# Kernel optimization log

Hardware: AMD Instinct MI355X
Metric: run time of the kernel (lower is better)

Reference implementation:

```python
import jax, jax.numpy as jnp
import numpy as np

TAU = 2.0     # membrane decay constant (init arg tau)
ALPHA = 1.0   # surrogate-gradient width (self.alpha() == 1.0)

# PiecewiseQuadratic surrogate spike: heaviside fwd, quadratic-band bwd
@jax.custom_vjp
def spike(v):
    return (v >= 0.0).astype(v.dtype)

def _spike_fwd(v):
    return spike(v), v

def _spike_bwd(v, g):
    sg = jnp.where(jnp.abs(v) > 1.0 / ALPHA, 0.0, -ALPHA * ALPHA * jnp.abs(v) + ALPHA)
    return (g * sg.astype(g.dtype),)

spike.defvjp(_spike_fwd, _spike_bwd)


def setup_inputs() -> dict:
    key = jax.random.key(0)
    x = jax.random.normal(key, (64, 64, 8192), dtype=jnp.float32)  # [B, T, F]
    return {
        "x": x,
        "momentum": jnp.array([0.9], dtype=jnp.float32),
        "lamb": jnp.array([0.5], dtype=jnp.float32),
        "thresholds": jnp.array([1.0], dtype=jnp.float32),
    }


def reference(x, momentum, lamb, thresholds):
    # regular=False -> lamb used directly (no sigmoid)
    mt = momentum[0]
    lb = lamb[0]
    th = thresholds[0]
    xt = jnp.moveaxis(x, 1, 0)  # [T, B, F] for scan over time
    u0 = jnp.zeros_like(xt[0])
    m0 = jnp.zeros_like(xt[0])

    def step(carry, xi):
        u_last, m = carry
        u = u_last / TAU + xi
        s = spike(u - th)
        m = mt * m + (1.0 - mt) * (u - u_last)
        u_next = (u * lb + m * (1.0 - lb)) * (1.0 - s)
        return (u_next, m), s

    _, out = jax.lax.scan(step, (u0, m0), xt)
    return jnp.moveaxis(out, 0, 1)  # [B, T, F]
```

## Files before the change

kernel.cpp:

```cpp
#include <hip/hip_runtime.h>


constexpr int B  = 64;
constexpr int T  = 64;
constexpr int F  = 8192;
constexpr int F2 = F / 2;
constexpr int P  = 4;

__global__ __launch_bounds__(256) void lif_fwd_kernel(
    const float2* __restrict__ x,
    const float*  __restrict__ momentum,
    const float*  __restrict__ lamb,
    const float*  __restrict__ thresholds,
    float2*       __restrict__ out)
{
#pragma clang fp contract(off)

    const int tid = blockIdx.x * blockDim.x + threadIdx.x;
    const int b   = tid / F2;
    const int f2  = tid - b * F2;

    const float mt  = momentum[0];
    const float omt = 1.0f - mt;
    const float lb  = lamb[0];
    const float olb = 1.0f - lb;
    const float th  = thresholds[0];

    const int base = b * (T * F2) + f2;

    float2 buf[P];
#pragma unroll
    for (int i = 0; i < P; ++i) buf[i] = x[base + i * F2];

    float u0 = 0.0f, u1 = 0.0f;
    float m0 = 0.0f, m1 = 0.0f;

    int load_idx  = base + P * F2;
    int store_idx = base;

#pragma unroll 4
    for (int t = 0; t < T; ++t) {
        const float2 xi = buf[t & (P - 1)];

        if (t + P < T) {
            buf[t & (P - 1)] = x[load_idx];
            load_idx += F2;
        }

        float2 sv;
        {
            const float u  = u0 * 0.5f + xi.x;
            const float s  = ((u - th) >= 0.0f) ? 1.0f : 0.0f;
            const float a  = mt * m0;
            const float bq = omt * (u - u0);
            m0 = a + bq;
            u0 = (u * lb + m0 * olb) * (1.0f - s);
            sv.x = s;
        }
        {
            const float u  = u1 * 0.5f + xi.y;
            const float s  = ((u - th) >= 0.0f) ? 1.0f : 0.0f;
            const float a  = mt * m1;
            const float bq = omt * (u - u1);
            m1 = a + bq;
            u1 = (u * lb + m1 * olb) * (1.0f - s);
            sv.y = s;
        }

        out[store_idx] = sv;
        store_idx += F2;
    }
}

extern "C" void kernel_launch(void* const* d_in, const int* in_sizes, int n_in,
                              void* d_out, int out_size, void* d_ws, size_t ws_size,
                              hipStream_t stream) {
    const float2* x   = (const float2*)d_in[0];
    const float*  mom = (const float*)d_in[1];
    const float*  lmb = (const float*)d_in[2];
    const float*  thr = (const float*)d_in[3];
    float2* out = (float2*)d_out;

    const int n_threads = B * F2;
    const int block = 256;
    const int grid = n_threads / block;
    lif_fwd_kernel<<<grid, block, 0, stream>>>(x, mom, lmb, thr, out);
}
```

Measured before the change: 242.7 us.

## Skew four batch chains per thread in staggered phases with nontemporal stores

Each thread now handles one feature across four batches. The four scan chains are offset in time by 16 steps and advanced in phased, fully unrolled loops, so independent recurrences interleave and more loads are in flight per thread. Accesses change from float2 to scalar float, and spike outputs are written with nontemporal stores to avoid polluting the cache. This cuts the thread count by a factor of four and raises register use, and scalar accesses may lower per-instruction memory efficiency.

```diff
diff --git a/kernel.cpp b/kernel.cpp
--- a/kernel.cpp
+++ b/kernel.cpp
@@ -1,24 +1,49 @@
 #include <hip/hip_runtime.h>
 
 
-constexpr int B  = 64;
-constexpr int T  = 64;
-constexpr int F  = 8192;
-constexpr int F2 = F / 2;
-constexpr int P  = 4;
+constexpr int B = 64;
+constexpr int T = 64;
+constexpr int F = 8192;
+constexpr int S   = 4;
+constexpr int DLT = 16;
+
+template <int GLO, int GHI>
+__device__ __forceinline__ void run_phase(
+    int tau0, const int* base, float* u, float* m,
+    const float* __restrict__ x, float* __restrict__ out,
+    float mt, float omt, float lb, float olb, float th)
+{
+#pragma clang fp contract(off)
+#pragma unroll
+    for (int k = 0; k < DLT; ++k) {
+        const int tau = tau0 + k;
+#pragma unroll
+        for (int g = GLO; g <= GHI; ++g) {
+            const int t   = tau - DLT * g;
+            const int idx = base[g] + t * F;
+            const float xv = x[idx];
+            const float uu = u[g] * 0.5f + xv;
+            const float s  = ((uu - th) >= 0.0f) ? 1.0f : 0.0f;
+            const float a  = mt * m[g];
+            const float bq = omt * (uu - u[g]);
+            m[g] = a + bq;
+            u[g] = (uu * lb + m[g] * olb) * (1.0f - s);
+            __builtin_nontemporal_store(s, &out[idx]);
+        }
+    }
+}
 
 __global__ __launch_bounds__(256) void lif_fwd_kernel(
-    const float2* __restrict__ x,
-    const float*  __restrict__ momentum,
-    const float*  __restrict__ lamb,
-    const float*  __restrict__ thresholds,
-    float2*       __restrict__ out)
+    const float* __restrict__ x,
+    const float* __restrict__ momentum,
+    const float* __restrict__ lamb,
+    const float* __restrict__ thresholds,
+    float*       __restrict__ out)
 {
 #pragma clang fp contract(off)
-
     const int tid = blockIdx.x * blockDim.x + threadIdx.x;
-    const int b   = tid / F2;
-    const int f2  = tid - b * F2;
+    const int b0  = tid >> 13;
+    const int f   = tid & (F - 1);
 
     const float mt  = momentum[0];
     const float omt = 1.0f - mt;
@@ -26,62 +51,34 @@
     const float olb = 1.0f - lb;
     const float th  = thresholds[0];
 
-    const int base = b * (T * F2) + f2;
+    int   base[S];
+    float u[S], m[S];
+#pragma unroll
+    for (int g = 0; g < S; ++g) {
+        base[g] = (b0 + 16 * g) * (T * F) + f;
+        u[g] = 0.0f;
+        m[g] = 0.0f;
+    }
 
-    float2 buf[P];
-#pragma unroll
-    for (int i = 0; i < P; ++i) buf[i] = x[base + i * F2];
-
-    float u0 = 0.0f, u1 = 0.0f;
-    float m0 = 0.0f, m1 = 0.0f;
-
-    int load_idx  = base + P * F2;
-    int store_idx = base;
-
-#pragma unroll 4
-    for (int t = 0; t < T; ++t) {
-        const float2 xi = buf[t & (P - 1)];
-
-        if (t + P < T) {
-            buf[t & (P - 1)] = x[load_idx];
-            load_idx += F2;
-        }
-
-        float2 sv;
-        {
-            const float u  = u0 * 0.5f + xi.x;
-            const float s  = ((u - th) >= 0.0f) ? 1.0f : 0.0f;
-            const float a  = mt * m0;
-            const float bq = omt * (u - u0);
-            m0 = a + bq;
-            u0 = (u * lb + m0 * olb) * (1.0f - s);
-            sv.x = s;
-        }
-        {
-            const float u  = u1 * 0.5f + xi.y;
-            const float s  = ((u - th) >= 0.0f) ? 1.0f : 0.0f;
-            const float a  = mt * m1;
-            const float bq = omt * (u - u1);
-            m1 = a + bq;
-            u1 = (u * lb + m1 * olb) * (1.0f - s);
-            sv.y = s;
-        }
-
-        out[store_idx] = sv;
-        store_idx += F2;
-    }
+    run_phase<0, 0>(  0, base, u, m, x, out, mt, omt, lb, olb, th);
+    run_phase<0, 1>( 16, base, u, m, x, out, mt, omt, lb, olb, th);
+    run_phase<0, 2>( 32, base, u, m, x, out, mt, omt, lb, olb, th);
+    run_phase<0, 3>( 48, base, u, m, x, out, mt, omt, lb, olb, th);
+    run_phase<1, 3>( 64, base, u, m, x, out, mt, omt, lb, olb, th);
+    run_phase<2, 3>( 80, base, u, m, x, out, mt, omt, lb, olb, th);
+    run_phase<3, 3>( 96, base, u, m, x, out, mt, omt, lb, olb, th);
 }
 
 extern "C" void kernel_launch(void* const* d_in, const int* in_sizes, int n_in,
                               void* d_out, int out_size, void* d_ws, size_t ws_size,
                               hipStream_t stream) {
-    const float2* x   = (const float2*)d_in[0];
-    const float*  mom = (const float*)d_in[1];
-    const float*  lmb = (const float*)d_in[2];
-    const float*  thr = (const float*)d_in[3];
-    float2* out = (float2*)d_out;
+    const float* x   = (const float*)d_in[0];
+    const float* mom = (const float*)d_in[1];
+    const float* lmb = (const float*)d_in[2];
+    const float* thr = (const float*)d_in[3];
+    float* out = (float*)d_out;
 
-    const int n_threads = B * F2;
+    const int n_threads = B * F / S;
     const int block = 256;
     const int grid = n_threads / block;
     lif_fwd_kernel<<<grid, block, 0, stream>>>(x, mom, lmb, thr, out);
```

New measurement: 240.3 us. About the same (-1.0%).
